# Performance work log

Hardware: AMD Instinct MI355X
Metric: run time of the kernel (lower is better)

The kernel has to match this reference:

```python
import jax, jax.numpy as jnp
import numpy as np

B, T, N, M, D = 4, 2, 2048, 2048, 3

def _pairwise_sq(a, b):
    # a: [B,N,D], b: [B,M,D] -> squared euclidean distances [B,N,M]
    a2 = jnp.sum(a * a, axis=-1)
    b2 = jnp.sum(b * b, axis=-1)
    ab = jnp.einsum('bnd,bmd->bnm', a, b)
    return jnp.maximum(a2[:, :, None] + b2[:, None, :] - 2.0 * ab, 0.0)


def setup_inputs() -> dict:
    key = jax.random.key(0)
    k1, k2, k3, k4 = jax.random.split(key, 4)
    x = jax.random.uniform(k1, (B, T, N, D), dtype=jnp.float32)
    # m_hat is the frozen motion model's output; small motions keep chamfer mask active
    m_hat = jax.random.uniform(k2, (B, 1, N, D), dtype=jnp.float32) * 0.02
    y_hat0 = jax.random.uniform(k3, (B, 1, M, D), dtype=jnp.float32)
    y_hat1 = jax.random.uniform(k4, (B, 1, M, D), dtype=jnp.float32)
    return {'x': x, 'm_hat': m_hat, 'y_hat0': y_hat0, 'y_hat1': y_hat1}


def reference(x, m_hat, y_hat0, y_hat1):
    sg = jax.lax.stop_gradient
    x_t0 = x[:, 0, :, :3]              # [B,N,3]
    x_t1 = x[:, 1, :, :3]              # [B,N,3]
    x_t1_hat = x_t0 + m_hat[:, 0]      # [B,N,3]

    # chamfer(x_t1_hat, x_t1): squared NN distances both ways
    d = _pairwise_sq(x_t1_hat, x_t1)   # [B,N,N]
    dist1 = jnp.min(d, axis=-1)
    dist2 = jnp.min(d, axis=-2)
    loss_chamfer = dist1.mean(axis=-1) + dist2.mean(axis=-1)          # [B]
    mask_chamfer = sg((loss_chamfer < 0.1).astype(x.dtype))[:, None, None, None]

    y0 = y_hat0[:, 0]                  # [B,M,3]
    dists = jnp.sqrt(_pairwise_sq(y0, x_t0))                          # [B,M,N]
    x_cat = jnp.concatenate([x_t0, x_t1], axis=1)                     # [B,2N,3]
    dists2 = jnp.sqrt(_pairwise_sq(y0, x_cat))                        # [B,M,2N]

    min_dists = jnp.min(dists, axis=-1)        # [B,M]
    min_indices = jnp.argmin(dists, axis=-1)   # [B,M]
    min_dists2 = jnp.min(dists2, axis=-1)      # [B,M]

    mask_dist = sg((min_dists < 0.05).astype(x.dtype))[:, None, :, None]      # [B,1,M,1]
    mask_dist_neg = sg((min_dists2 > 0.2).astype(x.dtype))[:, None, :, None]  # [B,1,M,1]

    nearest_m = jnp.take_along_axis(m_hat[:, 0], min_indices[:, :, None], axis=1)  # [B,M,3]

    # chamfer(x_t0, y_hat0): only dist1 used, masked mean over entries < 0.1
    c1 = jnp.min(_pairwise_sq(x_t0, y0), axis=-1)                     # [B,N]
    sel = c1 < 0.1
    loss_dist = jnp.sum(jnp.where(sel, c1, 0.0)) / jnp.maximum(jnp.sum(sel.astype(c1.dtype)), 1.0)

    pred = (y_hat1 - y_hat0) * mask_chamfer * mask_dist               # [B,1,M,3]
    tgt = nearest_m[:, None, :, :] * mask_chamfer * mask_dist
    loss_dynamic = jnp.mean((pred - tgt) ** 2)

    my_hat_static = (y_hat1 - y_hat0) * mask_dist_neg
    loss_static = jnp.mean(my_hat_static ** 2)

    return (loss_dynamic, loss_static, loss_dist)
```

## Files before the change

### kernel.cpp

```cpp
#include <hip/hip_runtime.h>
#include <math.h>

#define BATCH 4
#define NPTS  2048
#define NT    256
#define ROWS_PT 4
#define CPB     64
#define COLCHUNKS (NPTS / CPB)
#define ROWHALVES 2
#define ROWS_TOT  (BATCH * NPTS)
#define RB_BLOCKS (ROWS_TOT / 128)

#define OFF_PD1   0
#define OFF_PD2   (COLCHUNKS * ROWS_TOT)
#define OFF_PC1   (2 * COLCHUNKS * ROWS_TOT)
#define OFF_PRM3  (3 * COLCHUNKS * ROWS_TOT)
#define OFF_PRM2  (4 * COLCHUNKS * ROWS_TOT)
#define OFF_BLK   (6 * COLCHUNKS * ROWS_TOT)
#define OFF_CNT   (OFF_BLK + RB_BLOCKS * 32)

#define INF_BITS 0x7f800000u

typedef unsigned long long ull;

__device__ __forceinline__ float sqnorm3(float x, float y, float z) {
    return __fadd_rn(__fadd_rn(__fmul_rn(x, x), __fmul_rn(y, y)), __fmul_rn(z, z));
}

#define SRC_T0  0
#define SRC_T1  1
#define SRC_T1H 2
#define SRC_Y0  3

__device__ __forceinline__ float4 make_point(int src, bool col, int b, int i,
    const float* __restrict__ x, const float* __restrict__ m_hat,
    const float* __restrict__ y_hat0)
{
    float px, py, pz;
    if (src == SRC_Y0) {
        const float* p = y_hat0 + ((size_t)b * NPTS + i) * 3;
        px = p[0]; py = p[1]; pz = p[2];
    } else if (src == SRC_T1) {
        const float* p = x + ((size_t)(b * 2 + 1) * NPTS + i) * 3;
        px = p[0]; py = p[1]; pz = p[2];
    } else {
        const float* p = x + ((size_t)(b * 2 + 0) * NPTS + i) * 3;
        px = p[0]; py = p[1]; pz = p[2];
        if (src == SRC_T1H) {
            const float* mh = m_hat + ((size_t)b * NPTS + i) * 3;
            px += mh[0]; py += mh[1]; pz += mh[2];
        }
    }
    float w = sqnorm3(px, py, pz);
    if (col) { px *= -2.0f; py *= -2.0f; pz *= -2.0f; }
    return make_float4(px, py, pz, w);
}

__device__ __forceinline__ ull shfl_xor_u64(ull v, int m) {
    int lo = __shfl_xor((int)(v & 0xFFFFFFFFull), m);
    int hi = __shfl_xor((int)(v >> 32), m);
    return ((ull)(unsigned)hi << 32) | (unsigned)lo;
}

__global__ __launch_bounds__(NT) void pairwise_kernel(
    const float* __restrict__ x, const float* __restrict__ m_hat,
    const float* __restrict__ y_hat0, float* __restrict__ ws)
{
    __shared__ float4 tile[CPB];

    int tid = threadIdx.x;
    int rowHalf  = blockIdx.x >> 5;
    int colChunk = blockIdx.x & 31;
    int b    = blockIdx.y;
    int prob = blockIdx.z;

    if (blockIdx.x == 0 && b == 0 && prob == 0 && tid == 0)
        ((unsigned*)ws)[OFF_CNT] = 0u;

    int rsrc, csrc, outOff;
    switch (prob) {
        case 0:  rsrc = SRC_T1H; csrc = SRC_T1;  outOff = OFF_PD1;  break;
        case 1:  rsrc = SRC_T1;  csrc = SRC_T1H; outOff = OFF_PD2;  break;
        case 2:  rsrc = SRC_Y0;  csrc = SRC_T0;  outOff = -1;       break;
        case 3:  rsrc = SRC_Y0;  csrc = SRC_T1;  outOff = OFF_PRM3; break;
        default: rsrc = SRC_T0;  csrc = SRC_Y0;  outOff = OFF_PC1;  break;
    }

    int colBase = colChunk * CPB;
    if (tid < CPB) tile[tid] = make_point(csrc, true, b, colBase + tid, x, m_hat, y_hat0);

    int r0 = rowHalf * (NT * ROWS_PT) + tid;
    float4 a[ROWS_PT];
    #pragma unroll
    for (int k = 0; k < ROWS_PT; ++k)
        a[k] = make_point(rsrc, false, b, r0 + k * NT, x, m_hat, y_hat0);

    __syncthreads();

    if (prob == 2) {
        float best[ROWS_PT];
        int bestIdx[ROWS_PT];
        #pragma unroll
        for (int k = 0; k < ROWS_PT; ++k) { best[k] = __uint_as_float(INF_BITS); bestIdx[k] = 0; }
        #pragma unroll 4
        for (int c = 0; c < CPB; ++c) {
            float4 q = tile[c];
            #pragma unroll
            for (int k = 0; k < ROWS_PT; ++k) {
                float s = a[k].x * q.x + a[k].y * q.y + a[k].z * q.z;
                float u = __fadd_rn(a[k].w, q.w);
                float d = fmaxf(__fadd_rn(u, s), 0.0f);
                if (d < best[k]) { best[k] = d; bestIdx[k] = c; }
            }
        }
        ull* prm2 = (ull*)(ws + OFF_PRM2);
        #pragma unroll
        for (int k = 0; k < ROWS_PT; ++k) {
            ull key = ((ull)__float_as_uint(best[k]) << 32) |
                      (unsigned)(colBase + bestIdx[k]);
            prm2[(size_t)colChunk * ROWS_TOT + b * NPTS + r0 + k * NT] = key;
        }
    } else {
        float best[ROWS_PT];
        #pragma unroll
        for (int k = 0; k < ROWS_PT; ++k) best[k] = __uint_as_float(INF_BITS);
        #pragma unroll 4
        for (int c = 0; c < CPB; ++c) {
            float4 q = tile[c];
            #pragma unroll
            for (int k = 0; k < ROWS_PT; ++k) {
                float s = a[k].x * q.x + a[k].y * q.y + a[k].z * q.z;
                float u = __fadd_rn(a[k].w, q.w);
                float d = fmaxf(__fadd_rn(u, s), 0.0f);
                best[k] = fminf(best[k], d);
            }
        }
        #pragma unroll
        for (int k = 0; k < ROWS_PT; ++k)
            ws[outOff + (size_t)colChunk * ROWS_TOT + b * NPTS + r0 + k * NT] = best[k];
    }
}

__global__ __launch_bounds__(NT) void rowreduce_kernel(
    const float* __restrict__ m_hat, const float* __restrict__ y_hat0,
    const float* __restrict__ y_hat1, float* __restrict__ ws, float* __restrict__ out)
{
    int tid  = threadIdx.x;
    int row  = blockIdx.x * 128 + (tid >> 1);
    int half = tid & 1;
    int b    = row >> 11;

    const ull* prm2 = (const ull*)(ws + OFF_PRM2);

    float d1m = __uint_as_float(INF_BITS), d2m = d1m, c1m = d1m, r3m = d1m;
    ull k2 = ~0ull;
    #pragma unroll
    for (int c = 0; c < 16; ++c) {
        int idx = (half * 16 + c) * ROWS_TOT + row;
        d1m = fminf(d1m, ws[OFF_PD1 + idx]);
        d2m = fminf(d2m, ws[OFF_PD2 + idx]);
        c1m = fminf(c1m, ws[OFF_PC1 + idx]);
        r3m = fminf(r3m, ws[OFF_PRM3 + idx]);
        ull kk = prm2[idx];
        k2 = (kk < k2) ? kk : k2;
    }
    d1m = fminf(d1m, __shfl_xor(d1m, 1));
    d2m = fminf(d2m, __shfl_xor(d2m, 1));
    c1m = fminf(c1m, __shfl_xor(c1m, 1));
    r3m = fminf(r3m, __shfl_xor(r3m, 1));
    { ull o = shfl_xor_u64(k2, 1); k2 = (o < k2) ? o : k2; }

    float d2sq = __uint_as_float((unsigned)(k2 >> 32));
    unsigned idxm = (unsigned)(k2 & 0xFFFFFFFFull);
    float md   = (sqrtf(d2sq) < 0.05f) ? 1.0f : 0.0f;
    float dcat = fminf(d2sq, r3m);
    float mneg = (sqrtf(dcat) > 0.2f) ? 1.0f : 0.0f;

    const float* p0 = y_hat0 + (size_t)row * 3;
    const float* p1 = y_hat1 + (size_t)row * 3;
    const float* nm = m_hat + ((size_t)b * NPTS + idxm) * 3;

    float dyn = 0.f, stat = 0.f;
    #pragma unroll
    for (int k = 0; k < 3; ++k) {
        float diff = p1[k] - p0[k];
        float e = md * (diff - nm[k]);
        dyn += e * e;
        float s = mneg * diff;
        stat += s * s;
    }
    float cs = (c1m < 0.1f) ? c1m : 0.f;
    float cn = (c1m < 0.1f) ? 1.f  : 0.f;
    float s1 = d1m, s2 = d2m;
    if (half) { s1 = s2 = cs = cn = dyn = stat = 0.f; }

    #pragma unroll
    for (int off = 32; off > 0; off >>= 1) {
        s1  += __shfl_down(s1,  off);
        s2  += __shfl_down(s2,  off);
        cs  += __shfl_down(cs,  off);
        cn  += __shfl_down(cn,  off);
        dyn += __shfl_down(dyn, off);
        stat+= __shfl_down(stat,off);
    }
    __shared__ float sm[4][6];
    int wv = tid >> 6, ln = tid & 63;
    if (ln == 0) {
        sm[wv][0] = s1; sm[wv][1] = s2; sm[wv][2] = cs;
        sm[wv][3] = cn; sm[wv][4] = dyn; sm[wv][5] = stat;
    }
    __syncthreads();

    __shared__ int sLast;
    if (tid == 0) {
        #pragma unroll
        for (int j = 0; j < 6; ++j)
            ws[OFF_BLK + blockIdx.x * 32 + j] = sm[0][j] + sm[1][j] + sm[2][j] + sm[3][j];
        __threadfence();
        unsigned old = atomicAdd((unsigned*)ws + OFF_CNT, 1u);
        sLast = (old == RB_BLOCKS - 1) ? 1 : 0;
    }
    __syncthreads();
    if (!sLast) return;

    __threadfence();
    int lane = tid;
    if (lane < 64) {
        float v[6];
        #pragma unroll
        for (int j = 0; j < 6; ++j) v[j] = ws[OFF_BLK + lane * 32 + j];
        #pragma unroll
        for (int off = 8; off > 0; off >>= 1) {
            #pragma unroll
            for (int j = 0; j < 6; ++j) {
                float t = __shfl_down(v[j], off);
                if (((lane & 15) + off) < 16) v[j] += t;
            }
        }
        __shared__ float bs[4][6];
        if ((lane & 15) == 0) {
            #pragma unroll
            for (int j = 0; j < 6; ++j) bs[lane >> 4][j] = v[j];
        }
        __builtin_amdgcn_s_waitcnt(0);
        if (lane == 0) {
            float dyn = 0.f, stat = 0.f, cs = 0.f, cn = 0.f;
            for (int bb = 0; bb < 4; ++bb) {
                float lc = bs[bb][0] / (float)NPTS + bs[bb][1] / (float)NPTS;
                float maskc = (lc < 0.1f) ? 1.0f : 0.0f;
                dyn  += maskc * bs[bb][4];
                stat += bs[bb][5];
                cs   += bs[bb][2];
                cn   += bs[bb][3];
            }
            const float denom = (float)(BATCH * NPTS * 3);
            out[0] = dyn / denom;
            out[1] = stat / denom;
            out[2] = cs / fmaxf(cn, 1.0f);
        }
    }
}

extern "C" void kernel_launch(void* const* d_in, const int* in_sizes, int n_in,
                              void* d_out, int out_size, void* d_ws, size_t ws_size,
                              hipStream_t stream)
{
    const float* x      = (const float*)d_in[0];
    const float* m_hat  = (const float*)d_in[1];
    const float* y_hat0 = (const float*)d_in[2];
    const float* y_hat1 = (const float*)d_in[3];
    float* ws  = (float*)d_ws;
    float* out = (float*)d_out;

    pairwise_kernel<<<dim3(ROWHALVES * COLCHUNKS, BATCH, 5), dim3(NT), 0, stream>>>(
        x, m_hat, y_hat0, ws);
    rowreduce_kernel<<<dim3(RB_BLOCKS), dim3(NT), 0, stream>>>(
        m_hat, y_hat0, y_hat1, ws, out);
}
```

Before: 87.56 us.

## Reuse pairwise distance matrices for both row and column minima

Cuts the five pairwise-distance problems down to three by computing column-wise minima from the same matrix tiles used for row minima: the symmetric chamfer pair and the y0/x_t0 versus x_t0/y0 pair now share one distance evaluation each. Column minima are obtained by a per-column wave-wide shuffle reduction, a shared-memory combine across the four waves, and a second-stage reduce across row halves in the reduction kernel. This removes about 40% of the distance arithmetic but adds a 6-step shuffle reduction per column inside the inner loop and drops the explicit unroll pragmas. Because the shuffle chain is serial per column, it may offset the saved FLOPs.

```diff
diff --git a/kernel.cpp b/kernel.cpp
--- a/kernel.cpp
+++ b/kernel.cpp
@@ -11,12 +11,13 @@
 #define ROWS_TOT  (BATCH * NPTS)
 #define RB_BLOCKS (ROWS_TOT / 128)
 
+#define CH_R      (COLCHUNKS * ROWS_TOT)
 #define OFF_PD1   0
-#define OFF_PD2   (COLCHUNKS * ROWS_TOT)
-#define OFF_PC1   (2 * COLCHUNKS * ROWS_TOT)
-#define OFF_PRM3  (3 * COLCHUNKS * ROWS_TOT)
-#define OFF_PRM2  (4 * COLCHUNKS * ROWS_TOT)
-#define OFF_BLK   (6 * COLCHUNKS * ROWS_TOT)
+#define OFF_PRM3  CH_R
+#define OFF_PRM2  (2 * CH_R)
+#define OFF_PCA   (4 * CH_R)
+#define OFF_PCB   (OFF_PCA + 2 * ROWS_TOT)
+#define OFF_BLK   (OFF_PCB + 2 * ROWS_TOT)
 #define OFF_CNT   (OFF_BLK + RB_BLOCKS * 32)
 
 #define INF_BITS 0x7f800000u
@@ -62,28 +63,39 @@
     return ((ull)(unsigned)hi << 32) | (unsigned)lo;
 }
 
+__device__ __forceinline__ float wave_min(float v) {
+    #pragma unroll
+    for (int m = 1; m < 64; m <<= 1) v = fminf(v, __shfl_xor(v, m));
+    return v;
+}
+
+__device__ __forceinline__ float dist_sq(const float4& a, const float4& q) {
+    float s = a.x * q.x + a.y * q.y + a.z * q.z;
+    float u = __fadd_rn(a.w, q.w);
+    return fmaxf(__fadd_rn(u, s), 0.0f);
+}
+
 __global__ __launch_bounds__(NT) void pairwise_kernel(
     const float* __restrict__ x, const float* __restrict__ m_hat,
     const float* __restrict__ y_hat0, float* __restrict__ ws)
 {
     __shared__ float4 tile[CPB];
+    __shared__ float  cw[4][CPB];
 
     int tid = threadIdx.x;
     int rowHalf  = blockIdx.x >> 5;
     int colChunk = blockIdx.x & 31;
-    int b    = blockIdx.y;
-    int prob = blockIdx.z;
-
-    if (blockIdx.x == 0 && b == 0 && prob == 0 && tid == 0)
+    int b   = blockIdx.y;
+    int mat = blockIdx.z;
+
+    if (blockIdx.x == 0 && b == 0 && mat == 0 && tid == 0)
         ((unsigned*)ws)[OFF_CNT] = 0u;
 
-    int rsrc, csrc, outOff;
-    switch (prob) {
-        case 0:  rsrc = SRC_T1H; csrc = SRC_T1;  outOff = OFF_PD1;  break;
-        case 1:  rsrc = SRC_T1;  csrc = SRC_T1H; outOff = OFF_PD2;  break;
-        case 2:  rsrc = SRC_Y0;  csrc = SRC_T0;  outOff = -1;       break;
-        case 3:  rsrc = SRC_Y0;  csrc = SRC_T1;  outOff = OFF_PRM3; break;
-        default: rsrc = SRC_T0;  csrc = SRC_Y0;  outOff = OFF_PC1;  break;
+    int rsrc, csrc;
+    switch (mat) {
+        case 0:  rsrc = SRC_T1H; csrc = SRC_T1; break;
+        case 1:  rsrc = SRC_Y0;  csrc = SRC_T0; break;
+        default: rsrc = SRC_Y0;  csrc = SRC_T1; break;
     }
 
     int colBase = colChunk * CPB;
@@ -97,47 +109,71 @@
 
     __syncthreads();
 
-    if (prob == 2) {
+    int wv = tid >> 6;
+    size_t rowSlot = (size_t)colChunk * ROWS_TOT + b * NPTS + r0;
+    size_t colSlot = (size_t)rowHalf * ROWS_TOT + b * NPTS + colBase;
+
+    if (mat == 0) {
+        float best[ROWS_PT];
+        #pragma unroll
+        for (int k = 0; k < ROWS_PT; ++k) best[k] = __uint_as_float(INF_BITS);
+        for (int c = 0; c < CPB; ++c) {
+            float4 q = tile[c];
+            float d0 = dist_sq(a[0], q), d1 = dist_sq(a[1], q);
+            float d2 = dist_sq(a[2], q), d3 = dist_sq(a[3], q);
+            best[0] = fminf(best[0], d0); best[1] = fminf(best[1], d1);
+            best[2] = fminf(best[2], d2); best[3] = fminf(best[3], d3);
+            float colv = wave_min(fminf(fminf(d0, d1), fminf(d2, d3)));
+            if ((tid & 63) == 0) cw[wv][c] = colv;
+        }
+        #pragma unroll
+        for (int k = 0; k < ROWS_PT; ++k)
+            ws[OFF_PD1 + rowSlot + k * NT] = best[k];
+        __syncthreads();
+        if (tid < CPB)
+            ws[OFF_PCA + colSlot + tid] =
+                fminf(fminf(cw[0][tid], cw[1][tid]), fminf(cw[2][tid], cw[3][tid]));
+    } else if (mat == 1) {
         float best[ROWS_PT];
         int bestIdx[ROWS_PT];
         #pragma unroll
         for (int k = 0; k < ROWS_PT; ++k) { best[k] = __uint_as_float(INF_BITS); bestIdx[k] = 0; }
-        #pragma unroll 4
         for (int c = 0; c < CPB; ++c) {
             float4 q = tile[c];
-            #pragma unroll
-            for (int k = 0; k < ROWS_PT; ++k) {
-                float s = a[k].x * q.x + a[k].y * q.y + a[k].z * q.z;
-                float u = __fadd_rn(a[k].w, q.w);
-                float d = fmaxf(__fadd_rn(u, s), 0.0f);
-                if (d < best[k]) { best[k] = d; bestIdx[k] = c; }
-            }
+            float d0 = dist_sq(a[0], q), d1 = dist_sq(a[1], q);
+            float d2 = dist_sq(a[2], q), d3 = dist_sq(a[3], q);
+            if (d0 < best[0]) { best[0] = d0; bestIdx[0] = c; }
+            if (d1 < best[1]) { best[1] = d1; bestIdx[1] = c; }
+            if (d2 < best[2]) { best[2] = d2; bestIdx[2] = c; }
+            if (d3 < best[3]) { best[3] = d3; bestIdx[3] = c; }
+            float colv = wave_min(fminf(fminf(d0, d1), fminf(d2, d3)));
+            if ((tid & 63) == 0) cw[wv][c] = colv;
         }
         ull* prm2 = (ull*)(ws + OFF_PRM2);
         #pragma unroll
         for (int k = 0; k < ROWS_PT; ++k) {
             ull key = ((ull)__float_as_uint(best[k]) << 32) |
                       (unsigned)(colBase + bestIdx[k]);
-            prm2[(size_t)colChunk * ROWS_TOT + b * NPTS + r0 + k * NT] = key;
-        }
+            prm2[rowSlot + k * NT] = key;
+        }
+        __syncthreads();
+        if (tid < CPB)
+            ws[OFF_PCB + colSlot + tid] =
+                fminf(fminf(cw[0][tid], cw[1][tid]), fminf(cw[2][tid], cw[3][tid]));
     } else {
         float best[ROWS_PT];
         #pragma unroll
         for (int k = 0; k < ROWS_PT; ++k) best[k] = __uint_as_float(INF_BITS);
-        #pragma unroll 4
         for (int c = 0; c < CPB; ++c) {
             float4 q = tile[c];
-            #pragma unroll
-            for (int k = 0; k < ROWS_PT; ++k) {
-                float s = a[k].x * q.x + a[k].y * q.y + a[k].z * q.z;
-                float u = __fadd_rn(a[k].w, q.w);
-                float d = fmaxf(__fadd_rn(u, s), 0.0f);
-                best[k] = fminf(best[k], d);
-            }
+            best[0] = fminf(best[0], dist_sq(a[0], q));
+            best[1] = fminf(best[1], dist_sq(a[1], q));
+            best[2] = fminf(best[2], dist_sq(a[2], q));
+            best[3] = fminf(best[3], dist_sq(a[3], q));
         }
         #pragma unroll
         for (int k = 0; k < ROWS_PT; ++k)
-            ws[outOff + (size_t)colChunk * ROWS_TOT + b * NPTS + r0 + k * NT] = best[k];
+            ws[OFF_PRM3 + rowSlot + k * NT] = best[k];
     }
 }
 
@@ -152,21 +188,20 @@
 
     const ull* prm2 = (const ull*)(ws + OFF_PRM2);
 
-    float d1m = __uint_as_float(INF_BITS), d2m = d1m, c1m = d1m, r3m = d1m;
+    float d1m = __uint_as_float(INF_BITS), r3m = d1m;
     ull k2 = ~0ull;
     #pragma unroll
     for (int c = 0; c < 16; ++c) {
         int idx = (half * 16 + c) * ROWS_TOT + row;
         d1m = fminf(d1m, ws[OFF_PD1 + idx]);
-        d2m = fminf(d2m, ws[OFF_PD2 + idx]);
-        c1m = fminf(c1m, ws[OFF_PC1 + idx]);
         r3m = fminf(r3m, ws[OFF_PRM3 + idx]);
         ull kk = prm2[idx];
         k2 = (kk < k2) ? kk : k2;
     }
+    float d2m = fminf(ws[OFF_PCA + row], ws[OFF_PCA + ROWS_TOT + row]);
+    float c1m = fminf(ws[OFF_PCB + row], ws[OFF_PCB + ROWS_TOT + row]);
+
     d1m = fminf(d1m, __shfl_xor(d1m, 1));
-    d2m = fminf(d2m, __shfl_xor(d2m, 1));
-    c1m = fminf(c1m, __shfl_xor(c1m, 1));
     r3m = fminf(r3m, __shfl_xor(r3m, 1));
     { ull o = shfl_xor_u64(k2, 1); k2 = (o < k2) ? o : k2; }
 
@@ -272,7 +307,7 @@
     float* ws  = (float*)d_ws;
     float* out = (float*)d_out;
 
-    pairwise_kernel<<<dim3(ROWHALVES * COLCHUNKS, BATCH, 5), dim3(NT), 0, stream>>>(
+    pairwise_kernel<<<dim3(ROWHALVES * COLCHUNKS, BATCH, 3), dim3(NT), 0, stream>>>(
         x, m_hat, y_hat0, ws);
     rowreduce_kernel<<<dim3(RB_BLOCKS), dim3(NT), 0, stream>>>(
         m_hat, y_hat0, y_hat1, ws, out);
```

Result: slower. 92.34 us (+5.5%).
